# Kernel tuning notes

Hardware: AMD Instinct MI355X
Metric: run time of the kernel (lower is better)

## Reference

```python
import jax, jax.numpy as jnp
import numpy as np

H = 16  # num_heads


def setup_inputs() -> dict:
    key = jax.random.key(0)
    ks = jax.random.split(key, 9)
    L, N, E, I = 2048, 2, 2048, 2048
    s = 0.02
    return {
        "query": jax.random.normal(ks[0], (L, N, E), jnp.float32),
        "q_proj": jax.random.normal(ks[1], (I, E), jnp.float32) * s,
        "q_bias": jax.random.normal(ks[2], (I,), jnp.float32) * s,
        "k_proj": jax.random.normal(ks[3], (I, E), jnp.float32) * s,
        "k_bias": jax.random.normal(ks[4], (I,), jnp.float32) * s,
        "v_proj": jax.random.normal(ks[5], (I, E), jnp.float32) * s,
        "v_bias": jax.random.normal(ks[6], (I,), jnp.float32) * s,
        "out_proj": jax.random.normal(ks[7], (E, I), jnp.float32) * s,
        "out_bias": jax.random.normal(ks[8], (E,), jnp.float32) * s,
    }


def reference(query, q_proj, q_bias, k_proj, k_bias, v_proj, v_bias, out_proj, out_bias):
    L, N, E = query.shape
    h = H
    d = q_proj.shape[0] // h
    scale = d ** (-0.5)

    def split_heads(x):
        # [L, N, h*d] -> [N, h, L, d]  (matches view(L, N*h, d).transpose(0,1))
        return x.reshape(L, N, h, d).transpose(1, 2, 0, 3)

    q = split_heads(query @ q_proj.T + q_bias) * scale
    k = split_heads(query @ k_proj.T + k_bias)
    v = split_heads(query @ v_proj.T + v_bias)

    scores = jnp.einsum('nhld,nhkd->nhlk', q, k)  # [N, h, L, L]
    causal = jnp.tril(jnp.ones((L, L), dtype=bool))
    scores = jnp.where(causal, scores, jnp.float32(-10000.0))
    attn = jax.nn.softmax(scores, axis=-1)
    # dropout_p = 0.0 -> identity
    ctx = jnp.einsum('nhlk,nhkd->nhld', attn, v)
    ctx = ctx.transpose(2, 0, 1, 3).reshape(L, N, h * d)  # [L, N, h*d]
    return ctx @ out_proj.T + out_bias  # [L, N, E]
```

## Files before the change

### kernel.cpp

```cpp
#include <hip/hip_runtime.h>
#include <stdint.h>

#define L_SEQ 2048
#define NB 2
#define EMB 2048
#define II 2048
#define NH 16
#define DH 128
#define MROWS (L_SEQ * NB)

typedef __attribute__((ext_vector_type(8))) short bf16x8;
typedef __attribute__((ext_vector_type(4))) float f32x4;
typedef unsigned short u16;
typedef unsigned int u32;

__device__ __forceinline__ u16 f2bf(float f) {
  u32 u = __builtin_bit_cast(u32, f);
  u = u + 0x7fffu + ((u >> 16) & 1u);
  return (u16)(u >> 16);
}
__device__ __forceinline__ u16 f2bf_trunc(float f) {
  return (u16)(__builtin_bit_cast(u32, f) >> 16);
}

__device__ __forceinline__ void gl_lds16(const void* g, const u16* l) {
  __builtin_amdgcn_global_load_lds(
      (const __attribute__((address_space(1))) void*)(uintptr_t)g,
      (__attribute__((address_space(3))) void*)(u32)(uintptr_t)l, 16, 0, 0);
}

__global__ __launch_bounds__(256) void cast_all(
    const float* __restrict__ q, const float* __restrict__ w0, const float* __restrict__ w1,
    const float* __restrict__ w2, const float* __restrict__ w3, u16* __restrict__ dq,
    u16* __restrict__ dw) {
  const int b = blockIdx.x, t = threadIdx.x;
  const float* src;
  u16* dst;
  int idx;
  if (b < 8192) {
    src = q; dst = dq; idx = b * 256 + t;
  } else {
    int u = b - 8192;
    int sel = u >> 12;
    src = (sel == 0) ? w0 : (sel == 1) ? w1 : (sel == 2) ? w2 : w3;
    dst = dw + (size_t)sel * II * EMB;
    idx = (u & 4095) * 256 + t;
  }
  float4 v = ((const float4*)src)[idx];
  ushort4 o;
  o.x = f2bf(v.x); o.y = f2bf(v.y); o.z = f2bf(v.z); o.w = f2bf(v.w);
  ((ushort4*)dst)[idx] = o;
}

__global__ __launch_bounds__(256) void transpose_v(const u16* __restrict__ V,
                                                   u16* __restrict__ Vt) {
  __shared__ u16 tile[128][72];
  const int lb = blockIdx.x * 64;
  const int h = blockIdx.y;
  const u16* src = V + (size_t)h * L_SEQ * DH;
  u16* dst = Vt + (size_t)h * DH * L_SEQ;
  const int t = threadIdx.x;
  {
    const int l = t & 63, d0 = (t >> 6) * 32;
#pragma unroll
    for (int c = 0; c < 4; c++) {
      uint4 u = *(const uint4*)(src + (size_t)(lb + l) * DH + d0 + c * 8);
      const u16* e = (const u16*)&u;
#pragma unroll
      for (int x = 0; x < 8; x++) tile[d0 + c * 8 + x][l] = e[x];
    }
  }
  __syncthreads();
  {
    const int d = t >> 1, lc = (t & 1) * 32;
#pragma unroll
    for (int c = 0; c < 4; c++) {
      uint4 u = *(const uint4*)&tile[d][lc + c * 8];
      *(uint4*)(dst + (size_t)d * L_SEQ + lb + lc + c * 8) = u;
    }
  }
}

#define BK8 64
#define NT8 (EMB / BK8)

__global__ __launch_bounds__(512, 2) void gemm_qkv_8p(
    const u16* __restrict__ A, const u16* __restrict__ B, const float* __restrict__ qb,
    const float* __restrict__ kb, const float* __restrict__ vb, u16* __restrict__ out_bf,
    float qscale) {
  __shared__ __align__(16) u16 sm[2][32768];
  const int t = threadIdx.x;
  const int lane = t & 63, wv = t >> 6;
  const int quad = lane >> 4, l15 = lane & 15, x7 = l15 & 7;
  const int wm2 = wv >> 2, wn4 = wv & 3;
  const int srow = lane >> 3;
  const int schunk = (lane & 7) ^ (lane >> 3);

  const int bid = blockIdx.x;
  const int swz = (bid & 7) * 48 + (bid >> 3);
  const int bxx = swz >> 4;
  const int byy = swz & 15;
  const int n0 = bxx * 256, m0 = byy * 256;

  const u16* abase = A + (size_t)m0 * EMB;
  const u16* bbase = B + (size_t)n0 * EMB;

  auto stageA = [&](int buf, int k0, int u) {
    int row = u * 64 + wv * 8 + srow;
    const u16* dst = (buf ? sm[1] : sm[0]) + u * 4096 + wv * 512;
    gl_lds16(abase + (size_t)row * EMB + k0 + schunk * 8, dst);
  };
  auto stageB = [&](int buf, int k0, int u) {
    int row = u * 64 + wv * 8 + srow;
    const u16* dst = (buf ? sm[1] : sm[0]) + 16384 + u * 4096 + wv * 512;
    gl_lds16(bbase + (size_t)row * EMB + k0 + schunk * 8, dst);
  };

  stageA(0, 0, 0); stageA(0, 0, 2);
  stageB(0, 0, 0); stageB(0, 0, 1); stageB(0, 0, 2); stageB(0, 0, 3);
  stageA(0, 0, 1); stageA(0, 0, 3);
  stageA(1, BK8, 0); stageA(1, BK8, 2);
  __asm__ volatile("s_waitcnt vmcnt(4)" ::: "memory");
  __builtin_amdgcn_s_barrier();

  f32x4 acc[8][4] = {};
  bf16x8 afr[4][2];

#pragma unroll 1
  for (int tt = 0; tt < NT8; ++tt) {
    const int cb = tt & 1, nb_ = (tt + 1) & 1;
    const u16* cur = cb ? sm[1] : sm[0];
    const int kn1 = (tt + 1) * BK8;
    const int kn2 = (tt + 2) * BK8;
    const bool pf1 = (tt + 1 < NT8);
    const bool pf2 = (tt + 2 < NT8);

    {
#pragma unroll
      for (int mi = 0; mi < 4; mi++)
#pragma unroll
        for (int ks = 0; ks < 2; ks++)
          afr[mi][ks] =
              *(const bf16x8*)(cur + (wm2 * 128 + mi * 16 + l15) * 64 + (((ks * 4 + quad) ^ x7)) * 8);
      bf16x8 bfr2[2][2];
#pragma unroll
      for (int nj = 0; nj < 2; nj++)
#pragma unroll
        for (int ks = 0; ks < 2; ks++)
          bfr2[nj][ks] = *(const bf16x8*)(cur + 16384 + (wn4 * 64 + nj * 16 + l15) * 64 +
                                          (((ks * 4 + quad) ^ x7)) * 8);
      if (pf1) { stageB(nb_, kn1, 0); stageB(nb_, kn1, 1); stageB(nb_, kn1, 2); stageB(nb_, kn1, 3); }
      __builtin_amdgcn_s_barrier();
      __builtin_amdgcn_s_setprio(1);
#pragma unroll
      for (int ks = 0; ks < 2; ks++)
#pragma unroll
        for (int mi = 0; mi < 4; mi++)
#pragma unroll
          for (int nj = 0; nj < 2; nj++)
            acc[mi][nj] =
                __builtin_amdgcn_mfma_f32_16x16x32_bf16(afr[mi][ks], bfr2[nj][ks], acc[mi][nj], 0, 0, 0);
      __builtin_amdgcn_s_setprio(0);
      __builtin_amdgcn_s_barrier();
    }

    {
      bf16x8 bfr2[2][2];
#pragma unroll
      for (int nj = 0; nj < 2; nj++)
#pragma unroll
        for (int ks = 0; ks < 2; ks++)
          bfr2[nj][ks] = *(const bf16x8*)(cur + 16384 + (wn4 * 64 + (nj + 2) * 16 + l15) * 64 +
                                          (((ks * 4 + quad) ^ x7)) * 8);
      if (pf1) {
        stageA(nb_, kn1, 1); stageA(nb_, kn1, 3);
        __asm__ volatile("s_waitcnt vmcnt(8)" ::: "memory");
      } else {
        __asm__ volatile("s_waitcnt vmcnt(0)" ::: "memory");
      }
      __builtin_amdgcn_s_barrier();
      __builtin_amdgcn_s_setprio(1);
#pragma unroll
      for (int ks = 0; ks < 2; ks++)
#pragma unroll
        for (int mi = 0; mi < 4; mi++)
#pragma unroll
          for (int nj = 0; nj < 2; nj++)
            acc[mi][nj + 2] =
                __builtin_amdgcn_mfma_f32_16x16x32_bf16(afr[mi][ks], bfr2[nj][ks], acc[mi][nj + 2], 0, 0, 0);
      __builtin_amdgcn_s_setprio(0);
      __builtin_amdgcn_s_barrier();
    }

    {
#pragma unroll
      for (int mi = 0; mi < 4; mi++)
#pragma unroll
        for (int ks = 0; ks < 2; ks++)
          afr[mi][ks] = *(const bf16x8*)(cur + (wm2 * 128 + (mi + 4) * 16 + l15) * 64 +
                                         (((ks * 4 + quad) ^ x7)) * 8);
      bf16x8 bfr2[2][2];
#pragma unroll
      for (int nj = 0; nj < 2; nj++)
#pragma unroll
        for (int ks = 0; ks < 2; ks++)
          bfr2[nj][ks] = *(const bf16x8*)(cur + 16384 + (wn4 * 64 + nj * 16 + l15) * 64 +
                                          (((ks * 4 + quad) ^ x7)) * 8);
      if (pf2) { stageA(cb, kn2, 0); stageA(cb, kn2, 2); }
      __builtin_amdgcn_s_barrier();
      __builtin_amdgcn_s_setprio(1);
#pragma unroll
      for (int ks = 0; ks < 2; ks++)
#pragma unroll
        for (int mi = 0; mi < 4; mi++)
#pragma unroll
          for (int nj = 0; nj < 2; nj++)
            acc[mi + 4][nj] =
                __builtin_amdgcn_mfma_f32_16x16x32_bf16(afr[mi][ks], bfr2[nj][ks], acc[mi + 4][nj], 0, 0, 0);
      __builtin_amdgcn_s_setprio(0);
      __builtin_amdgcn_s_barrier();
    }

    {
      bf16x8 bfr2[2][2];
#pragma unroll
      for (int nj = 0; nj < 2; nj++)
#pragma unroll
        for (int ks = 0; ks < 2; ks++)
          bfr2[nj][ks] = *(const bf16x8*)(cur + 16384 + (wn4 * 64 + (nj + 2) * 16 + l15) * 64 +
                                          (((ks * 4 + quad) ^ x7)) * 8);
      if (pf2) {
        __asm__ volatile("s_waitcnt vmcnt(4)" ::: "memory");
      } else if (pf1) {
        __asm__ volatile("s_waitcnt vmcnt(2)" ::: "memory");
      }
      __builtin_amdgcn_s_barrier();
      __builtin_amdgcn_s_setprio(1);
#pragma unroll
      for (int ks = 0; ks < 2; ks++)
#pragma unroll
        for (int mi = 0; mi < 4; mi++)
#pragma unroll
          for (int nj = 0; nj < 2; nj++)
            acc[mi + 4][nj + 2] =
                __builtin_amdgcn_mfma_f32_16x16x32_bf16(afr[mi][ks], bfr2[nj][ks], acc[mi + 4][nj + 2], 0, 0, 0);
      __builtin_amdgcn_s_setprio(0);
      __builtin_amdgcn_s_barrier();
    }
  }

  const int mat = n0 >> 11;
  const float* bp = (mat == 0) ? qb : (mat == 1) ? kb : vb;
  const float sc2 = (mat == 0) ? qscale : 1.0f;
#pragma unroll
  for (int mi = 0; mi < 8; mi++) {
#pragma unroll
    for (int nj = 0; nj < 4; nj++) {
#pragma unroll
      for (int r = 0; r < 4; r++) {
        int row = m0 + wm2 * 128 + mi * 16 + quad * 4 + r;
        int col = n0 + wn4 * 64 + nj * 16 + l15;
        int cc = col & 2047;
        float v = (acc[mi][nj][r] + bp[cc]) * sc2;
        int l = row >> 1, nb = row & 1;
        int hh = cc >> 7, dd = cc & 127;
        out_bf[(size_t)mat * MROWS * II + ((size_t)(nb * NH + hh) * L_SEQ + l) * DH + dd] =
            f2bf(v);
      }
    }
  }
}

__global__ __launch_bounds__(256) void gemm_nt(
    const u16* __restrict__ A, const u16* __restrict__ B, const float* __restrict__ b0,
    const float* __restrict__ b1, const float* __restrict__ b2, u16* __restrict__ out_bf,
    float* __restrict__ out_f, int Nd, int K, float qscale, int mode) {
  __shared__ __align__(16) u16 a_sm[128 * 64];
  __shared__ __align__(16) u16 b_sm[128 * 64];
  const int t = threadIdx.x;
  const int lane = t & 63, wv = t >> 6;
  const int quad = lane >> 4, l15 = lane & 15;
  const int x7 = l15 & 7;
  const int wm = (wv >> 1) * 64, wn = (wv & 1) * 64;
  const int m0 = blockIdx.y * 128, n0 = blockIdx.x * 128;
  const int srow = lane >> 3;
  const int schunk = (lane & 7) ^ (lane >> 3);

  f32x4 acc[4][4] = {};
  const u16* abase = A + (size_t)m0 * K;
  const u16* bbase = B + (size_t)n0 * K;

  for (int k0 = 0; k0 < K; k0 += 64) {
    __syncthreads();
#pragma unroll
    for (int j = 0; j < 4; j++) {
      int ci = wv * 4 + j;
      int row = ci * 8 + srow;
      gl_lds16(abase + (size_t)row * K + k0 + schunk * 8, a_sm + ci * 512);
      gl_lds16(bbase + (size_t)row * K + k0 + schunk * 8, b_sm + ci * 512);
    }
    __syncthreads();
#pragma unroll
    for (int ks = 0; ks < 2; ks++) {
      bf16x8 af[4], bfr[4];
#pragma unroll
      for (int i = 0; i < 4; i++)
        af[i] = *(const bf16x8*)(a_sm + (wm + i * 16 + l15) * 64 + ((ks * 4 + quad) ^ x7) * 8);
#pragma unroll
      for (int j = 0; j < 4; j++)
        bfr[j] = *(const bf16x8*)(b_sm + (wn + j * 16 + l15) * 64 + ((ks * 4 + quad) ^ x7) * 8);
#pragma unroll
      for (int i = 0; i < 4; i++)
#pragma unroll
        for (int j = 0; j < 4; j++)
          acc[i][j] = __builtin_amdgcn_mfma_f32_16x16x32_bf16(af[i], bfr[j], acc[i][j], 0, 0, 0);
    }
  }

  const int mat = n0 >> 11;
  const float* bp = (mode == 1) ? b0 : (mat == 0 ? b0 : (mat == 1 ? b1 : b2));
  const float sc2 = (mode == 0 && mat == 0) ? qscale : 1.0f;
#pragma unroll
  for (int i = 0; i < 4; i++) {
#pragma unroll
    for (int j = 0; j < 4; j++) {
#pragma unroll
      for (int r = 0; r < 4; r++) {
        int row = m0 + wm + i * 16 + quad * 4 + r;
        int col = n0 + wn + j * 16 + l15;
        if (mode == 0) {
          int cc = col & 2047;
          float v = (acc[i][j][r] + bp[cc]) * sc2;
          int l = row >> 1, nb = row & 1;
          int hh = cc >> 7, dd = cc & 127;
          out_bf[(size_t)mat * MROWS * II + ((size_t)(nb * NH + hh) * L_SEQ + l) * DH + dd] =
              f2bf(v);
        } else {
          out_f[(size_t)row * Nd + col] = acc[i][j][r] + bp[col];
        }
      }
    }
  }
}

__global__ __launch_bounds__(256, 2) void flash_attn(
    const u16* __restrict__ Qh, const u16* __restrict__ Kh, const u16* __restrict__ Vt,
    u16* __restrict__ ctx) {
  __shared__ __align__(16) u16 k_sm[2][64 * 128];
  __shared__ __align__(16) u16 v_sm[2][128 * 64];
  const int bx = blockIdx.x;
  const int nh = ((bx & 7) << 2) | ((bx >> 3) & 3);
  const int g = (bx >> 5) & 7;
  const int qt = (bx < 256) ? (15 - g) : g;
  const int q0 = qt * 128;
  const int nK = 2 * (qt + 1);
  const int t = threadIdx.x;
  const int lane = t & 63, wv = t >> 6;
  const int quad = lane >> 4, l15 = lane & 15;
  const int x7 = l15 & 7;
  const size_t hq = (size_t)nh * L_SEQ * DH;
  const u16* qp = Qh + hq;
  const u16* kp = Kh + hq;
  const u16* vp = Vt + hq;
  const int n = nh >> 4, h = nh & 15;
  const int srow = lane >> 4;
  const int spos = lane & 15;
  const int vrow = lane >> 3;
  const int vpos = lane & 7;

  auto stageKV = [&](int bb, int kb) {
#pragma unroll
    for (int i = 0; i < 4; i++) {
      int ci = wv * 4 + i;
      int krow = ci * 4 + srow;
      int gck = spos ^ (krow & 7);
      gl_lds16(kp + (size_t)(kb + krow) * DH + gck * 8,
               (bb ? k_sm[1] : k_sm[0]) + ci * 512);
      int drow = ci * 8 + vrow;
      int gcv = vpos ^ (drow & 7);
      gl_lds16(vp + (size_t)drow * L_SEQ + kb + gcv * 8,
               (bb ? v_sm[1] : v_sm[0]) + ci * 512);
    }
  };

  bf16x8 qf[2][4];
#pragma unroll
  for (int mi = 0; mi < 2; mi++)
#pragma unroll
    for (int ks = 0; ks < 4; ks++)
      qf[mi][ks] = *(const bf16x8*)(qp + (size_t)(q0 + wv * 32 + mi * 16 + l15) * DH +
                                    ks * 32 + quad * 8);

  f32x4 o_acc[2][8] = {};
  float l_part[2][4] = {};

  stageKV(0, 0);

#pragma unroll 1
  for (int jb = 0; jb < nK; jb++) {
    const int b = jb & 1;
    const u16* kbuf = b ? k_sm[1] : k_sm[0];
    const u16* vbuf = b ? v_sm[1] : v_sm[0];
    u16* pwb = (b ? k_sm[1] : k_sm[0]) + wv * 2048;
    const int kb = jb * 64;

    __syncthreads();
    if (jb + 1 < nK) stageKV(b ^ 1, kb + 64);

    f32x4 s[2][4] = {};
    __builtin_amdgcn_s_setprio(1);
#pragma unroll
    for (int nt = 0; nt < 4; nt++) {
#pragma unroll
      for (int ks = 0; ks < 4; ks++) {
        bf16x8 kf = *(const bf16x8*)(kbuf + (nt * 16 + l15) * 128 + ((ks * 4 + quad) ^ x7) * 8);
#pragma unroll
        for (int mi = 0; mi < 2; mi++)
          s[mi][nt] = __builtin_amdgcn_mfma_f32_16x16x32_bf16(qf[mi][ks], kf, s[mi][nt], 0, 0, 0);
      }
    }
    __builtin_amdgcn_s_setprio(0);

    __asm__ volatile("s_waitcnt lgkmcnt(0)" ::: "memory");
    __builtin_amdgcn_sched_barrier(0);
    __builtin_amdgcn_s_barrier();
    __builtin_amdgcn_sched_barrier(0);

    const bool diag = (jb >= nK - 2);
#pragma unroll
    for (int mi = 0; mi < 2; mi++) {
      const int rowg = q0 + wv * 32 + mi * 16 + quad * 4;
#pragma unroll
      for (int nt = 0; nt < 4; nt++) {
        const int colg = kb + nt * 16 + l15;
#pragma unroll
        for (int r = 0; r < 4; r++) {
          float p = __builtin_amdgcn_exp2f(s[mi][nt][r]);
          if (diag && colg > rowg + r) p = 0.f;
          l_part[mi][r] += p;
          int pr = mi * 16 + quad * 4 + r;
          int chunk = nt * 2 + (l15 >> 3);
          int pos = chunk ^ (pr & 7);
          pwb[pr * 64 + pos * 8 + (l15 & 7)] = f2bf_trunc(p);
        }
      }
    }
    __asm__ volatile("s_waitcnt lgkmcnt(0)" ::: "memory");
    __builtin_amdgcn_sched_barrier(0);

    bf16x8 pf[2][2];
#pragma unroll
    for (int mi = 0; mi < 2; mi++)
#pragma unroll
      for (int ks = 0; ks < 2; ks++)
        pf[mi][ks] = *(const bf16x8*)(pwb + (mi * 16 + l15) * 64 + ((ks * 4 + quad) ^ x7) * 8);
    __builtin_amdgcn_s_setprio(1);
#pragma unroll
    for (int nt = 0; nt < 8; nt++) {
#pragma unroll
      for (int ks = 0; ks < 2; ks++) {
        bf16x8 vf = *(const bf16x8*)(vbuf + (nt * 16 + l15) * 64 + ((ks * 4 + quad) ^ x7) * 8);
#pragma unroll
        for (int mi = 0; mi < 2; mi++)
          o_acc[mi][nt] =
              __builtin_amdgcn_mfma_f32_16x16x32_bf16(pf[mi][ks], vf, o_acc[mi][nt], 0, 0, 0);
      }
    }
    __builtin_amdgcn_s_setprio(0);
  }

#pragma unroll
  for (int mi = 0; mi < 2; mi++) {
#pragma unroll
    for (int r = 0; r < 4; r++) {
      float lv = l_part[mi][r];
#pragma unroll
      for (int off = 1; off < 16; off <<= 1) lv += __shfl_xor(lv, off, 64);
      float inv = 1.f / lv;
      const int lrow = q0 + wv * 32 + mi * 16 + quad * 4 + r;
#pragma unroll
      for (int nt = 0; nt < 8; nt++) {
        int dd = nt * 16 + l15;
        ctx[((size_t)lrow * NB + n) * EMB + h * DH + dd] = f2bf(o_acc[mi][nt][r] * inv);
      }
    }
  }
}

extern "C" void kernel_launch(void* const* d_in, const int* in_sizes, int n_in,
                              void* d_out, int out_size, void* d_ws, size_t ws_size,
                              hipStream_t stream) {
  const float* query    = (const float*)d_in[0];
  const float* q_proj   = (const float*)d_in[1];
  const float* q_bias   = (const float*)d_in[2];
  const float* k_proj   = (const float*)d_in[3];
  const float* k_bias   = (const float*)d_in[4];
  const float* v_proj   = (const float*)d_in[5];
  const float* v_bias   = (const float*)d_in[6];
  const float* out_proj = (const float*)d_in[7];
  const float* out_bias = (const float*)d_in[8];

  u16* ws  = (u16*)d_ws;
  u16* Xbf = ws;
  u16* Wq  = Xbf + (size_t)MROWS * EMB;
  u16* Wk  = Wq + (size_t)II * EMB;
  u16* Wv  = Wk + (size_t)II * EMB;
  u16* Wo  = Wv + (size_t)II * EMB;
  u16* Qw  = Wo + (size_t)EMB * II;
  u16* Kw  = Qw + (size_t)MROWS * II;
  u16* Vw  = Kw + (size_t)MROWS * II;
  u16* Cw  = Vw + (size_t)MROWS * II;
  u16* Vtb = Xbf;

  cast_all<<<8192 + 4 * 4096, 256, 0, stream>>>(query, q_proj, k_proj, v_proj, out_proj,
                                                Xbf, Wq);

  const float qscale = 0.08838834764831845f * 1.4426950408889634f;
  gemm_qkv_8p<<<384, 512, 0, stream>>>(Xbf, Wq, q_bias, k_bias, v_bias, Qw, qscale);

  transpose_v<<<dim3(L_SEQ / 64, NB * NH), 256, 0, stream>>>(Vw, Vtb);

  flash_attn<<<512, 256, 0, stream>>>(Qw, Kw, Vtb, Cw);

  gemm_nt<<<dim3(EMB / 128, MROWS / 128), 256, 0, stream>>>(
      Cw, Wo, out_bias, nullptr, nullptr, nullptr, (float*)d_out, EMB, II, 1.0f, 1);
}
```

Measured before the change: 400.6 us.

## Replace QKV and output GEMMs with shared 128x256 kernel using triple-buffered B prefetch

The two GEMM kernels become one templated-by-mode kernel that uses 128x256 tiles with 512 threads, a double-buffered A tile and a triple-buffered B tile, and prefetches two k-steps ahead. The QKV projection moves from 256x256 tiles on 384 blocks to 128x256 tiles on 768 blocks. The output projection moves from the simple synchronous 128x128 gemm_nt to the same pipelined kernel on 256 blocks. The aim is to deepen the load pipeline, lift occupancy or wave count for the QKV GEMM, and replace the unpipelined output GEMM. The cost is less register reuse per tile in the QKV GEMM and more LDS per block.

Result: faster. 369.9 us (-7.7%).

```diff
diff --git a/kernel.cpp b/kernel.cpp
--- a/kernel.cpp
+++ b/kernel.cpp
@@ -81,14 +81,15 @@
   }
 }
 
-#define BK8 64
-#define NT8 (EMB / BK8)
-
-__global__ __launch_bounds__(512, 2) void gemm_qkv_8p(
-    const u16* __restrict__ A, const u16* __restrict__ B, const float* __restrict__ qb,
-    const float* __restrict__ kb, const float* __restrict__ vb, u16* __restrict__ out_bf,
-    float qscale) {
-  __shared__ __align__(16) u16 sm[2][32768];
+#define BK2 64
+#define NT2 (EMB / BK2)
+
+__global__ __launch_bounds__(512, 2) void gemm_2p(
+    const u16* __restrict__ A, const u16* __restrict__ B, const float* __restrict__ b0,
+    const float* __restrict__ b1, const float* __restrict__ b2, u16* __restrict__ out_bf,
+    float* __restrict__ out_f, float qscale, int mode) {
+  __shared__ __align__(16) u16 a_sm[2][8192];
+  __shared__ __align__(16) u16 b_sm[3][16384];
   const int t = threadIdx.x;
   const int lane = t & 63, wv = t >> 6;
   const int quad = lane >> 4, l15 = lane & 15, x7 = l15 & 7;
@@ -97,59 +98,61 @@
   const int schunk = (lane & 7) ^ (lane >> 3);
 
   const int bid = blockIdx.x;
-  const int swz = (bid & 7) * 48 + (bid >> 3);
-  const int bxx = swz >> 4;
-  const int byy = swz & 15;
-  const int n0 = bxx * 256, m0 = byy * 256;
+  const int cpx = gridDim.x >> 3;
+  const int swz = (bid & 7) * cpx + (bid >> 3);
+  const int byy = swz & 31;
+  const int bxx = swz >> 5;
+  const int m0 = byy * 128, n0 = bxx * 256;
 
   const u16* abase = A + (size_t)m0 * EMB;
   const u16* bbase = B + (size_t)n0 * EMB;
 
   auto stageA = [&](int buf, int k0, int u) {
     int row = u * 64 + wv * 8 + srow;
-    const u16* dst = (buf ? sm[1] : sm[0]) + u * 4096 + wv * 512;
+    const u16* dst = (buf ? a_sm[1] : a_sm[0]) + u * 4096 + wv * 512;
     gl_lds16(abase + (size_t)row * EMB + k0 + schunk * 8, dst);
   };
   auto stageB = [&](int buf, int k0, int u) {
     int row = u * 64 + wv * 8 + srow;
-    const u16* dst = (buf ? sm[1] : sm[0]) + 16384 + u * 4096 + wv * 512;
+    const u16* dst = (buf == 0 ? b_sm[0] : buf == 1 ? b_sm[1] : b_sm[2]) + u * 4096 + wv * 512;
     gl_lds16(bbase + (size_t)row * EMB + k0 + schunk * 8, dst);
   };
 
-  stageA(0, 0, 0); stageA(0, 0, 2);
   stageB(0, 0, 0); stageB(0, 0, 1); stageB(0, 0, 2); stageB(0, 0, 3);
-  stageA(0, 0, 1); stageA(0, 0, 3);
-  stageA(1, BK8, 0); stageA(1, BK8, 2);
-  __asm__ volatile("s_waitcnt vmcnt(4)" ::: "memory");
+  stageA(0, 0, 0); stageA(0, 0, 1);
+  stageB(1, BK2, 0); stageB(1, BK2, 1); stageB(1, BK2, 2); stageB(1, BK2, 3);
+  stageA(1, BK2, 0); stageA(1, BK2, 1);
+  __asm__ volatile("s_waitcnt vmcnt(0)" ::: "memory");
   __builtin_amdgcn_s_barrier();
 
-  f32x4 acc[8][4] = {};
-  bf16x8 afr[4][2];
+  f32x4 acc[4][4] = {};
+  int tB = 0;
 
 #pragma unroll 1
-  for (int tt = 0; tt < NT8; ++tt) {
-    const int cb = tt & 1, nb_ = (tt + 1) & 1;
-    const u16* cur = cb ? sm[1] : sm[0];
-    const int kn1 = (tt + 1) * BK8;
-    const int kn2 = (tt + 2) * BK8;
-    const bool pf1 = (tt + 1 < NT8);
-    const bool pf2 = (tt + 2 < NT8);
+  for (int tt = 0; tt < NT2; ++tt) {
+    const u16* aC = (tt & 1) ? a_sm[1] : a_sm[0];
+    const u16* bC = (tB == 0) ? b_sm[0] : (tB == 1) ? b_sm[1] : b_sm[2];
+    const int tB2 = (tB + 2 >= 3) ? tB - 1 : tB + 2;
+    const int kk2 = (tt + 2) * BK2;
+    const bool pf2 = (tt + 2 < NT2);
+
+    bf16x8 afr[4][2];
 
     {
 #pragma unroll
       for (int mi = 0; mi < 4; mi++)
 #pragma unroll
         for (int ks = 0; ks < 2; ks++)
-          afr[mi][ks] =
-              *(const bf16x8*)(cur + (wm2 * 128 + mi * 16 + l15) * 64 + (((ks * 4 + quad) ^ x7)) * 8);
-      bf16x8 bfr2[2][2];
+          afr[mi][ks] = *(const bf16x8*)(aC + wm2 * 4096 + (mi * 16 + l15) * 64 +
+                                         ((ks * 4 + quad) ^ x7) * 8);
+      bf16x8 bfr[2][2];
 #pragma unroll
       for (int nj = 0; nj < 2; nj++)
 #pragma unroll
         for (int ks = 0; ks < 2; ks++)
-          bfr2[nj][ks] = *(const bf16x8*)(cur + 16384 + (wn4 * 64 + nj * 16 + l15) * 64 +
-                                          (((ks * 4 + quad) ^ x7)) * 8);
-      if (pf1) { stageB(nb_, kn1, 0); stageB(nb_, kn1, 1); stageB(nb_, kn1, 2); stageB(nb_, kn1, 3); }
+          bfr[nj][ks] = *(const bf16x8*)(bC + wn4 * 4096 + (nj * 16 + l15) * 64 +
+                                         ((ks * 4 + quad) ^ x7) * 8);
+      if (pf2) { stageB(tB2, kk2, 0); stageB(tB2, kk2, 1); stageB(tB2, kk2, 2); stageB(tB2, kk2, 3); }
       __builtin_amdgcn_s_barrier();
       __builtin_amdgcn_s_setprio(1);
 #pragma unroll
@@ -159,23 +162,23 @@
 #pragma unroll
           for (int nj = 0; nj < 2; nj++)
             acc[mi][nj] =
-                __builtin_amdgcn_mfma_f32_16x16x32_bf16(afr[mi][ks], bfr2[nj][ks], acc[mi][nj], 0, 0, 0);
+                __builtin_amdgcn_mfma_f32_16x16x32_bf16(afr[mi][ks], bfr[nj][ks], acc[mi][nj], 0, 0, 0);
       __builtin_amdgcn_s_setprio(0);
       __builtin_amdgcn_s_barrier();
     }
 
     {
-      bf16x8 bfr2[2][2];
+      bf16x8 bfr[2][2];
 #pragma unroll
       for (int nj = 0; nj < 2; nj++)
 #pragma unroll
         for (int ks = 0; ks < 2; ks++)
-          bfr2[nj][ks] = *(const bf16x8*)(cur + 16384 + (wn4 * 64 + (nj + 2) * 16 + l15) * 64 +
-                                          (((ks * 4 + quad) ^ x7)) * 8);
-      if (pf1) {
-        stageA(nb_, kn1, 1); stageA(nb_, kn1, 3);
-        __asm__ volatile("s_waitcnt vmcnt(8)" ::: "memory");
-      } else {
+          bfr[nj][ks] = *(const bf16x8*)(bC + wn4 * 4096 + ((nj + 2) * 16 + l15) * 64 +
+                                         ((ks * 4 + quad) ^ x7) * 8);
+      if (pf2) {
+        stageA(tt & 1, kk2, 0); stageA(tt & 1, kk2, 1);
+        __asm__ volatile("s_waitcnt vmcnt(6)" ::: "memory");
+      } else if (tt == NT2 - 2) {
         __asm__ volatile("s_waitcnt vmcnt(0)" ::: "memory");
       }
       __builtin_amdgcn_s_barrier();
@@ -187,156 +190,45 @@
 #pragma unroll
           for (int nj = 0; nj < 2; nj++)
             acc[mi][nj + 2] =
-                __builtin_amdgcn_mfma_f32_16x16x32_bf16(afr[mi][ks], bfr2[nj][ks], acc[mi][nj + 2], 0, 0, 0);
+                __builtin_amdgcn_mfma_f32_16x16x32_bf16(afr[mi][ks], bfr[nj][ks], acc[mi][nj + 2], 0, 0, 0);
       __builtin_amdgcn_s_setprio(0);
       __builtin_amdgcn_s_barrier();
     }
 
-    {
-#pragma unroll
-      for (int mi = 0; mi < 4; mi++)
-#pragma unroll
-        for (int ks = 0; ks < 2; ks++)
-          afr[mi][ks] = *(const bf16x8*)(cur + (wm2 * 128 + (mi + 4) * 16 + l15) * 64 +
-                                         (((ks * 4 + quad) ^ x7)) * 8);
-      bf16x8 bfr2[2][2];
-#pragma unroll
-      for (int nj = 0; nj < 2; nj++)
-#pragma unroll
-        for (int ks = 0; ks < 2; ks++)
-          bfr2[nj][ks] = *(const bf16x8*)(cur + 16384 + (wn4 * 64 + nj * 16 + l15) * 64 +
-                                          (((ks * 4 + quad) ^ x7)) * 8);
-      if (pf2) { stageA(cb, kn2, 0); stageA(cb, kn2, 2); }
-      __builtin_amdgcn_s_barrier();
-      __builtin_amdgcn_s_setprio(1);
-#pragma unroll
-      for (int ks = 0; ks < 2; ks++)
-#pragma unroll
-        for (int mi = 0; mi < 4; mi++)
-#pragma unroll
-          for (int nj = 0; nj < 2; nj++)
-            acc[mi + 4][nj] =
-                __builtin_amdgcn_mfma_f32_16x16x32_bf16(afr[mi][ks], bfr2[nj][ks], acc[mi + 4][nj], 0, 0, 0);
-      __builtin_amdgcn_s_setprio(0);
-      __builtin_amdgcn_s_barrier();
-    }
-
-    {
-      bf16x8 bfr2[2][2];
-#pragma unroll
-      for (int nj = 0; nj < 2; nj++)
-#pragma unroll
-        for (int ks = 0; ks < 2; ks++)
-          bfr2[nj][ks] = *(const bf16x8*)(cur + 16384 + (wn4 * 64 + (nj + 2) * 16 + l15) * 64 +
-                                          (((ks * 4 + quad) ^ x7)) * 8);
-      if (pf2) {
-        __asm__ volatile("s_waitcnt vmcnt(4)" ::: "memory");
-      } else if (pf1) {
-        __asm__ volatile("s_waitcnt vmcnt(2)" ::: "memory");
-      }
-      __builtin_amdgcn_s_barrier();
-      __builtin_amdgcn_s_setprio(1);
-#pragma unroll
-      for (int ks = 0; ks < 2; ks++)
-#pragma unroll
-        for (int mi = 0; mi < 4; mi++)
-#pragma unroll
-          for (int nj = 0; nj < 2; nj++)
-            acc[mi + 4][nj + 2] =
-                __builtin_amdgcn_mfma_f32_16x16x32_bf16(afr[mi][ks], bfr2[nj][ks], acc[mi + 4][nj + 2], 0, 0, 0);
-      __builtin_amdgcn_s_setprio(0);
-      __builtin_amdgcn_s_barrier();
-    }
-  }
-
-  const int mat = n0 >> 11;
-  const float* bp = (mat == 0) ? qb : (mat == 1) ? kb : vb;
-  const float sc2 = (mat == 0) ? qscale : 1.0f;
-#pragma unroll
-  for (int mi = 0; mi < 8; mi++) {
-#pragma unroll
-    for (int nj = 0; nj < 4; nj++) {
-#pragma unroll
-      for (int r = 0; r < 4; r++) {
-        int row = m0 + wm2 * 128 + mi * 16 + quad * 4 + r;
-        int col = n0 + wn4 * 64 + nj * 16 + l15;
-        int cc = col & 2047;
-        float v = (acc[mi][nj][r] + bp[cc]) * sc2;
-        int l = row >> 1, nb = row & 1;
-        int hh = cc >> 7, dd = cc & 127;
-        out_bf[(size_t)mat * MROWS * II + ((size_t)(nb * NH + hh) * L_SEQ + l) * DH + dd] =
-            f2bf(v);
-      }
-    }
-  }
-}
-
-__global__ __launch_bounds__(256) void gemm_nt(
-    const u16* __restrict__ A, const u16* __restrict__ B, const float* __restrict__ b0,
-    const float* __restrict__ b1, const float* __restrict__ b2, u16* __restrict__ out_bf,
-    float* __restrict__ out_f, int Nd, int K, float qscale, int mode) {
-  __shared__ __align__(16) u16 a_sm[128 * 64];
-  __shared__ __align__(16) u16 b_sm[128 * 64];
-  const int t = threadIdx.x;
-  const int lane = t & 63, wv = t >> 6;
-  const int quad = lane >> 4, l15 = lane & 15;
-  const int x7 = l15 & 7;
-  const int wm = (wv >> 1) * 64, wn = (wv & 1) * 64;
-  const int m0 = blockIdx.y * 128, n0 = blockIdx.x * 128;
-  const int srow = lane >> 3;
-  const int schunk = (lane & 7) ^ (lane >> 3);
-
-  f32x4 acc[4][4] = {};
-  const u16* abase = A + (size_t)m0 * K;
-  const u16* bbase = B + (size_t)n0 * K;
-
-  for (int k0 = 0; k0 < K; k0 += 64) {
-    __syncthreads();
-#pragma unroll
-    for (int j = 0; j < 4; j++) {
-      int ci = wv * 4 + j;
-      int row = ci * 8 + srow;
-      gl_lds16(abase + (size_t)row * K + k0 + schunk * 8, a_sm + ci * 512);
-      gl_lds16(bbase + (size_t)row * K + k0 + schunk * 8, b_sm + ci * 512);
-    }
-    __syncthreads();
-#pragma unroll
-    for (int ks = 0; ks < 2; ks++) {
-      bf16x8 af[4], bfr[4];
-#pragma unroll
-      for (int i = 0; i < 4; i++)
-        af[i] = *(const bf16x8*)(a_sm + (wm + i * 16 + l15) * 64 + ((ks * 4 + quad) ^ x7) * 8);
-#pragma unroll
-      for (int j = 0; j < 4; j++)
-        bfr[j] = *(const bf16x8*)(b_sm + (wn + j * 16 + l15) * 64 + ((ks * 4 + quad) ^ x7) * 8);
-#pragma unroll
-      for (int i = 0; i < 4; i++)
-#pragma unroll
-        for (int j = 0; j < 4; j++)
-          acc[i][j] = __builtin_amdgcn_mfma_f32_16x16x32_bf16(af[i], bfr[j], acc[i][j], 0, 0, 0);
-    }
-  }
-
-  const int mat = n0 >> 11;
-  const float* bp = (mode == 1) ? b0 : (mat == 0 ? b0 : (mat == 1 ? b1 : b2));
-  const float sc2 = (mode == 0 && mat == 0) ? qscale : 1.0f;
-#pragma unroll
-  for (int i = 0; i < 4; i++) {
-#pragma unroll
-    for (int j = 0; j < 4; j++) {
-#pragma unroll
-      for (int r = 0; r < 4; r++) {
-        int row = m0 + wm + i * 16 + quad * 4 + r;
-        int col = n0 + wn + j * 16 + l15;
-        if (mode == 0) {
+    tB = (tB + 1 == 3) ? 0 : tB + 1;
+  }
+
+  if (mode == 0) {
+    const int mat = n0 >> 11;
+    const float* bp = (mat == 0) ? b0 : (mat == 1) ? b1 : b2;
+    const float sc2 = (mat == 0) ? qscale : 1.0f;
+#pragma unroll
+    for (int mi = 0; mi < 4; mi++) {
+#pragma unroll
+      for (int nj = 0; nj < 4; nj++) {
+#pragma unroll
+        for (int r = 0; r < 4; r++) {
+          int row = m0 + wm2 * 64 + mi * 16 + quad * 4 + r;
+          int col = n0 + wn4 * 64 + nj * 16 + l15;
           int cc = col & 2047;
-          float v = (acc[i][j][r] + bp[cc]) * sc2;
+          float v = (acc[mi][nj][r] + bp[cc]) * sc2;
           int l = row >> 1, nb = row & 1;
           int hh = cc >> 7, dd = cc & 127;
           out_bf[(size_t)mat * MROWS * II + ((size_t)(nb * NH + hh) * L_SEQ + l) * DH + dd] =
               f2bf(v);
-        } else {
-          out_f[(size_t)row * Nd + col] = acc[i][j][r] + bp[col];
+        }
+      }
+    }
+  } else {
+#pragma unroll
+    for (int mi = 0; mi < 4; mi++) {
+#pragma unroll
+      for (int nj = 0; nj < 4; nj++) {
+#pragma unroll
+        for (int r = 0; r < 4; r++) {
+          int row = m0 + wm2 * 64 + mi * 16 + quad * 4 + r;
+          int col = n0 + wn4 * 64 + nj * 16 + l15;
+          out_f[(size_t)row * EMB + col] = acc[mi][nj][r] + b0[col];
         }
       }
     }
@@ -516,12 +408,12 @@
                                                 Xbf, Wq);
 
   const float qscale = 0.08838834764831845f * 1.4426950408889634f;
-  gemm_qkv_8p<<<384, 512, 0, stream>>>(Xbf, Wq, q_bias, k_bias, v_bias, Qw, qscale);
+  gemm_2p<<<768, 512, 0, stream>>>(Xbf, Wq, q_bias, k_bias, v_bias, Qw, nullptr, qscale, 0);
 
   transpose_v<<<dim3(L_SEQ / 64, NB * NH), 256, 0, stream>>>(Vw, Vtb);
 
   flash_attn<<<512, 256, 0, stream>>>(Qw, Kw, Vtb, Cw);
 
-  gemm_nt<<<dim3(EMB / 128, MROWS / 128), 256, 0, stream>>>(
-      Cw, Wo, out_bias, nullptr, nullptr, nullptr, (float*)d_out, EMB, II, 1.0f, 1);
-}
+  gemm_2p<<<256, 512, 0, stream>>>(Cw, Wo, out_bias, nullptr, nullptr, nullptr,
+                                   (float*)d_out, 1.0f, 1);
+}
```
